# Optimization experiments

Hardware: AMD Instinct MI355X
Metric: run time of the kernel (lower is better)

Reference implementation:

```python
import jax, jax.numpy as jnp
import numpy as np

EPS = 1e-8  # torch F.cosine_similarity denominator clamp
MARGIN = 0.1  # default M in forward signature


def setup_inputs() -> dict:
    key = jax.random.key(0)
    k1, k2 = jax.random.split(key)
    N, B, D = 4096, 1, 1024
    wsi = jax.random.normal(k1, (N, B, D), dtype=jnp.float32)
    omic = jax.random.normal(k2, (N, B, D), dtype=jnp.float32)
    return {"wsi_embeddings": wsi, "omic_embeddings": omic}


def reference(wsi_embeddings, omic_embeddings):
    # [N, B=1, D] -> [N, D]
    W = wsi_embeddings[:, 0, :]
    O = omic_embeddings[:, 0, :]
    nw = jnp.linalg.norm(W, axis=-1)  # [N]
    no = jnp.linalg.norm(O, axis=-1)  # [N]
    # Full pairwise cosine similarity: S[i, j] = cos(wsi_i, omic_j)
    S = (W @ O.T) / jnp.maximum(nw[:, None] * no[None, :], EPS)  # [N, N]
    d = jnp.diagonal(S)  # cos(wsi_i, omic_i), the "self" similarity
    # off-diagonal hinge: relu(M - cos_ij + cos_ii); diagonal: 1 - cos_ii
    off = jax.nn.relu(MARGIN - S + d[:, None])
    eye = jnp.eye(S.shape[0], dtype=bool)
    L = jnp.where(eye, 1.0 - S, off)
    return jnp.mean(L)
```

## Files before the change

kernel.cpp:

```cpp
#include <hip/hip_runtime.h>
#include <stdint.h>

#define N 4096
#define D 1024
#define MARGIN 0.1f
#define BM 128
#define BN 128
#define BKB 128
#define QS 500.0f
#define INVQS2 (1.0f / (QS * QS))

typedef __attribute__((ext_vector_type(4))) int i32x4;

__global__ __launch_bounds__(256) void prep_kernel(
    const float* __restrict__ W, const float* __restrict__ O,
    uint8_t* __restrict__ Wn, uint8_t* __restrict__ On,
    float* __restrict__ dvec, float* __restrict__ out) {
  const int wv = threadIdx.x >> 6, ln = threadIdx.x & 63;
  const int row = blockIdx.x * 4 + wv;
  if (blockIdx.x == 0 && threadIdx.x == 0) *out = 0.0f;
  const float4* Wr = (const float4*)(W + (size_t)row * D);
  const float4* Or = (const float4*)(O + (size_t)row * D);
  float4 w[4], o[4];
  float sw = 0.f, so = 0.f, sd = 0.f;
  #pragma unroll
  for (int c = 0; c < 4; ++c) {
    w[c] = Wr[ln + c * 64];
    o[c] = Or[ln + c * 64];
    sw += w[c].x * w[c].x + w[c].y * w[c].y + w[c].z * w[c].z + w[c].w * w[c].w;
    so += o[c].x * o[c].x + o[c].y * o[c].y + o[c].z * o[c].z + o[c].w * o[c].w;
    sd += w[c].x * o[c].x + w[c].y * o[c].y + w[c].z * o[c].z + w[c].w * o[c].w;
  }
  #pragma unroll
  for (int off = 1; off < 64; off <<= 1) {
    sw += __shfl_xor(sw, off, 64);
    so += __shfl_xor(so, off, 64);
    sd += __shfl_xor(sd, off, 64);
  }
  const float inw = 1.0f / sqrtf(sw) * QS;
  const float ino = 1.0f / sqrtf(so) * QS;
  if (ln == 0) dvec[row] = sd * inw * ino * INVQS2;
  int* Wo = (int*)(Wn + (size_t)row * D);
  int* Oo = (int*)(On + (size_t)row * D);
  #pragma unroll
  for (int c = 0; c < 4; ++c) {
    int q0 = __float2int_rn(fminf(fmaxf(w[c].x * inw, -127.f), 127.f));
    int q1 = __float2int_rn(fminf(fmaxf(w[c].y * inw, -127.f), 127.f));
    int q2 = __float2int_rn(fminf(fmaxf(w[c].z * inw, -127.f), 127.f));
    int q3 = __float2int_rn(fminf(fmaxf(w[c].w * inw, -127.f), 127.f));
    Wo[ln + c * 64] = (q0 & 255) | ((q1 & 255) << 8) | ((q2 & 255) << 16) |
                      ((q3 & 255) << 24);
    q0 = __float2int_rn(fminf(fmaxf(o[c].x * ino, -127.f), 127.f));
    q1 = __float2int_rn(fminf(fmaxf(o[c].y * ino, -127.f), 127.f));
    q2 = __float2int_rn(fminf(fmaxf(o[c].z * ino, -127.f), 127.f));
    q3 = __float2int_rn(fminf(fmaxf(o[c].w * ino, -127.f), 127.f));
    Oo[ln + c * 64] = (q0 & 255) | ((q1 & 255) << 8) | ((q2 & 255) << 16) |
                      ((q3 & 255) << 24);
  }
}

__global__ __launch_bounds__(256) void gemm_loss_kernel(
    const uint8_t* __restrict__ Wn, const uint8_t* __restrict__ On,
    const float* __restrict__ dvec, float* __restrict__ out) {
  __shared__ __align__(16) uint8_t ldsA[BM * BKB];
  __shared__ __align__(16) uint8_t ldsB[BN * BKB];
  const int bx = blockIdx.x, by = blockIdx.y;
  const int t = threadIdx.x;
  const int wv = t >> 6, ln = t & 63;
  const int wm = wv >> 1, wn = wv & 1;
  const int lrow = ln & 15;
  const int quad = ln >> 4;
  const int l7 = lrow & 7;

  i32x4 acc[4][4] = {};

  const uint8_t* Ag = Wn + (size_t)(by * BM) * D;
  const uint8_t* Bg = On + (size_t)(bx * BN) * D;

  for (int kt = 0; kt < D / BKB; ++kt) {
    #pragma unroll
    for (int c = 0; c < 4; ++c) {
      const int g = c * 256 + t;
      const int r = g >> 3;
      const int gi = g & 7;
      const int col = (gi ^ (r & 7)) << 4;
      __builtin_amdgcn_global_load_lds(
          (const __attribute__((address_space(1))) void*)(Ag + (size_t)r * D + kt * BKB + col),
          (__attribute__((address_space(3))) void*)(ldsA + g * 16), 16, 0, 0);
      __builtin_amdgcn_global_load_lds(
          (const __attribute__((address_space(1))) void*)(Bg + (size_t)r * D + kt * BKB + col),
          (__attribute__((address_space(3))) void*)(ldsB + g * 16), 16, 0, 0);
    }
    __syncthreads();
    #pragma unroll
    for (int kk = 0; kk < 2; ++kk) {
      const int s0 = ((kk * 4 + quad) ^ l7) << 4;
      i32x4 aF[4], bF[4];
      #pragma unroll
      for (int mi = 0; mi < 4; ++mi) {
        const int rr = wm * 64 + mi * 16 + lrow;
        aF[mi] = *(const i32x4*)(ldsA + rr * BKB + s0);
      }
      #pragma unroll
      for (int ni = 0; ni < 4; ++ni) {
        const int cc = wn * 64 + ni * 16 + lrow;
        bF[ni] = *(const i32x4*)(ldsB + cc * BKB + s0);
      }
      #pragma unroll
      for (int mi = 0; mi < 4; ++mi)
        #pragma unroll
        for (int ni = 0; ni < 4; ++ni)
          acc[mi][ni] = __builtin_amdgcn_mfma_i32_16x16x64_i8(
              aF[mi], bF[ni], acc[mi][ni], 0, 0, 0);
    }
    __syncthreads();
  }

  float lsum = 0.0f;
  #pragma unroll
  for (int mi = 0; mi < 4; ++mi) {
    const int gibase = by * BM + wm * 64 + mi * 16 + quad * 4;
    #pragma unroll
    for (int r = 0; r < 4; ++r) {
      const int gi = gibase + r;
      const float di = dvec[gi];
      #pragma unroll
      for (int ni = 0; ni < 4; ++ni) {
        const int gj = bx * BN + wn * 64 + ni * 16 + lrow;
        const float s = (float)acc[mi][ni][r] * INVQS2;
        lsum += (gi == gj) ? (1.0f - s) : fmaxf(MARGIN - s + di, 0.0f);
      }
    }
  }
  #pragma unroll
  for (int off = 32; off; off >>= 1) lsum += __shfl_down(lsum, off, 64);
  __shared__ float bsum[4];
  if (ln == 0) bsum[wv] = lsum;
  __syncthreads();
  if (t == 0) {
    const float tot = (bsum[0] + bsum[1] + bsum[2] + bsum[3]) *
                      (1.0f / ((float)N * (float)N));
    atomicAdd(out, tot);
  }
}

extern "C" void kernel_launch(void* const* d_in, const int* in_sizes, int n_in,
                              void* d_out, int out_size, void* d_ws, size_t ws_size,
                              hipStream_t stream) {
  const float* W = (const float*)d_in[0];
  const float* O = (const float*)d_in[1];
  uint8_t* Wn = (uint8_t*)d_ws;
  uint8_t* On = Wn + (size_t)N * D;
  float* dvec = (float*)(On + (size_t)N * D);
  float* out = (float*)d_out;

  prep_kernel<<<N / 4, 256, 0, stream>>>(W, O, Wn, On, dvec, out);
  dim3 grid(N / BN, N / BM);
  gemm_loss_kernel<<<grid, 256, 0, stream>>>(Wn, On, dvec, out);
}
```

Baseline: 105.2 us.

## Double-buffer LDS tiles to overlap global loads with MFMA compute

Splits the shared-memory A/B tiles into two buffers and prefetches the next K-slice via global_load_lds while MFMAs consume the current one. The aim is to hide global-to-LDS latency behind compute instead of serialising load, sync and compute in each K iteration. LDS use doubles to 64KB per block, which may lower occupancy. The barrier sits after compute, and it is unclear whether the async LDS loads are waited on correctly before the other buffer is read.

```diff
diff --git a/kernel.cpp b/kernel.cpp
--- a/kernel.cpp
+++ b/kernel.cpp
@@ -62,8 +62,10 @@
 __global__ __launch_bounds__(256) void gemm_loss_kernel(
     const uint8_t* __restrict__ Wn, const uint8_t* __restrict__ On,
     const float* __restrict__ dvec, float* __restrict__ out) {
-  __shared__ __align__(16) uint8_t ldsA[BM * BKB];
-  __shared__ __align__(16) uint8_t ldsB[BN * BKB];
+  __shared__ __align__(16) uint8_t ldsA0[BM * BKB];
+  __shared__ __align__(16) uint8_t ldsB0[BN * BKB];
+  __shared__ __align__(16) uint8_t ldsA1[BM * BKB];
+  __shared__ __align__(16) uint8_t ldsB1[BN * BKB];
   const int bx = blockIdx.x, by = blockIdx.y;
   const int t = threadIdx.x;
   const int wv = t >> 6, ln = t & 63;
@@ -77,42 +79,60 @@
   const uint8_t* Ag = Wn + (size_t)(by * BM) * D;
   const uint8_t* Bg = On + (size_t)(bx * BN) * D;
 
-  for (int kt = 0; kt < D / BKB; ++kt) {
-    #pragma unroll
-    for (int c = 0; c < 4; ++c) {
-      const int g = c * 256 + t;
-      const int r = g >> 3;
-      const int gi = g & 7;
-      const int col = (gi ^ (r & 7)) << 4;
-      __builtin_amdgcn_global_load_lds(
-          (const __attribute__((address_space(1))) void*)(Ag + (size_t)r * D + kt * BKB + col),
-          (__attribute__((address_space(3))) void*)(ldsA + g * 16), 16, 0, 0);
-      __builtin_amdgcn_global_load_lds(
-          (const __attribute__((address_space(1))) void*)(Bg + (size_t)r * D + kt * BKB + col),
-          (__attribute__((address_space(3))) void*)(ldsB + g * 16), 16, 0, 0);
-    }
+#define STAGE(dstA, dstB, ktv) do {                                          \
+    _Pragma("unroll")                                                        \
+    for (int c_ = 0; c_ < 4; ++c_) {                                         \
+      const int g_ = c_ * 256 + t;        \
+      const int r_ = g_ >> 3;             \
+      const int gi_ = g_ & 7;                   \
+      const int col_ = (gi_ ^ (r_ & 7)) << 4;  \
+      __builtin_amdgcn_global_load_lds(                                      \
+          (const __attribute__((address_space(1))) void*)(                   \
+              Ag + (size_t)r_ * D + (ktv) * BKB + col_),                     \
+          (__attribute__((address_space(3))) void*)((dstA) + g_ * 16),       \
+          16, 0, 0);                                                         \
+      __builtin_amdgcn_global_load_lds(                                      \
+          (const __attribute__((address_space(1))) void*)(                   \
+              Bg + (size_t)r_ * D + (ktv) * BKB + col_),                     \
+          (__attribute__((address_space(3))) void*)((dstB) + g_ * 16),       \
+          16, 0, 0);                                                         \
+    }                                                                        \
+  } while (0)
+
+#define COMPUTE(srcA, srcB) do {                                             \
+    _Pragma("unroll")                                                        \
+    for (int kk = 0; kk < 2; ++kk) {       \
+           \
+      const int s0 = ((kk * 4 + quad) ^ l7) << 4;                            \
+      i32x4 aF[4], bF[4];                                                    \
+      _Pragma("unroll")                                                      \
+      for (int mi = 0; mi < 4; ++mi) {                                       \
+        const int rr = wm * 64 + mi * 16 + lrow;                             \
+        aF[mi] = *(const i32x4*)((srcA) + rr * BKB + s0);                    \
+      }                                                                      \
+      _Pragma("unroll")                                                      \
+      for (int ni = 0; ni < 4; ++ni) {                                       \
+        const int cc = wn * 64 + ni * 16 + lrow;                             \
+        bF[ni] = *(const i32x4*)((srcB) + cc * BKB + s0);                    \
+      }                                                                      \
+      _Pragma("unroll")                                                      \
+      for (int mi = 0; mi < 4; ++mi)                                         \
+        _Pragma("unroll")                                                    \
+        for (int ni = 0; ni < 4; ++ni)                                       \
+          acc[mi][ni] = __builtin_amdgcn_mfma_i32_16x16x64_i8(               \
+              aF[mi], bF[ni], acc[mi][ni], 0, 0, 0);                         \
+    }                                                                        \
+  } while (0)
+
+  STAGE(ldsA0, ldsB0, 0);
+  __syncthreads();
+  #pragma unroll
+  for (int kp = 0; kp < 4; ++kp) {
+    STAGE(ldsA1, ldsB1, kp * 2 + 1);
+    COMPUTE(ldsA0, ldsB0);
     __syncthreads();
-    #pragma unroll
-    for (int kk = 0; kk < 2; ++kk) {
-      const int s0 = ((kk * 4 + quad) ^ l7) << 4;
-      i32x4 aF[4], bF[4];
-      #pragma unroll
-      for (int mi = 0; mi < 4; ++mi) {
-        const int rr = wm * 64 + mi * 16 + lrow;
-        aF[mi] = *(const i32x4*)(ldsA + rr * BKB + s0);
-      }
-      #pragma unroll
-      for (int ni = 0; ni < 4; ++ni) {
-        const int cc = wn * 64 + ni * 16 + lrow;
-        bF[ni] = *(const i32x4*)(ldsB + cc * BKB + s0);
-      }
-      #pragma unroll
-      for (int mi = 0; mi < 4; ++mi)
-        #pragma unroll
-        for (int ni = 0; ni < 4; ++ni)
-          acc[mi][ni] = __builtin_amdgcn_mfma_i32_16x16x64_i8(
-              aF[mi], bF[ni], acc[mi][ni], 0, 0, 0);
-    }
+    if (kp < 3) STAGE(ldsA0, ldsB0, kp * 2 + 2);
+    COMPUTE(ldsA1, ldsB1);
     __syncthreads();
   }
 
```

After: 103.0 us. 1.02x faster.
